# Performance work log

Measured on AMD Instinct MI355X. Metric: run time of the kernel, lower is better.

## Reference

```python
import jax, jax.numpy as jnp
import numpy as np
from jax import lax

DN = ('NCHW', 'OIHW', 'NCHW')
NUM_CODES = 8192


def _conv(x, w, b):
    # Conv2d(k=4, s=2, p=1)
    y = lax.conv_general_dilated(x, w, (2, 2), ((1, 1), (1, 1)), dimension_numbers=DN)
    return y + b[None, :, None, None]


def _convT(x, w, b):
    # ConvTranspose2d(k=4, s=2, p=1) as lhs-dilated conv; kernel already in equivalent OIHW layout
    y = lax.conv_general_dilated(x, w, (1, 1), ((2, 2), (2, 2)), lhs_dilation=(2, 2), dimension_numbers=DN)
    return y + b[None, :, None, None]


def _aff(x, s, b):
    # eval-mode BatchNorm folded to per-channel affine
    return x * s[None, :, None, None] + b[None, :, None, None]


def _forward(x, ew1, eb1, bn1s, bn1b, ew2, eb2, bn2s, bn2b, ew3, eb3, bn3s, bn3b, ew4, eb4, embed, cluster_size, dw1, db1, dbn1s, dbn1b, dw2, db2, dbn2s, dbn2b, dw3, db3, dbn3s, dbn3b, dw4, db4):
    sg = lax.stop_gradient
    embed = sg(embed)          # codebook is a torch buffer -> no grad
    cluster_size = sg(cluster_size)
    relu = jax.nn.relu
    # ---- Encoder: 4 stride-2 convs ----
    h = relu(_aff(_conv(x, ew1, eb1), bn1s, bn1b))
    h = relu(_aff(_conv(h, ew2, eb2), bn2s, bn2b))
    h = relu(_aff(_conv(h, ew3, eb3), bn3s, bn3b))
    z = _conv(h, ew4, eb4)                       # [B, D, G, G]
    zt = jnp.transpose(z, (0, 2, 3, 1))          # [B, G, G, D]
    D = zt.shape[-1]
    flat = zt.reshape(-1, D)                     # [N, D]
    N = flat.shape[0]
    # ---- VQ: pairwise squared distance + argmin codebook lookup ----
    dist = (flat * flat).sum(1, keepdims=True) - 2.0 * (flat @ embed.T) + (embed * embed).sum(1)[None, :]
    soft = jax.nn.softmax(-dist, axis=-1)        # temperature = 1.0
    codes = jnp.argmin(dist, axis=1)             # [N]
    zq = embed[codes]                            # [N, D]
    commitment_loss = jnp.mean((flat - sg(zq)) ** 2)
    codebook_loss = jnp.mean((zq - sg(flat)) ** 2)
    avg_soft = soft.mean(0)
    usage_entropy = -(avg_soft * jnp.log(avg_soft + 1e-10)).sum()
    diversity_loss = -usage_entropy / float(np.log(NUM_CODES))
    zq_st = flat + sg(zq - flat)                 # straight-through estimator
    zq_grid = jnp.transpose(zq_st.reshape(zt.shape), (0, 3, 1, 2))  # [B, D, G, G]
    # ---- Decoder: 4 stride-2 transposed convs ----
    h = relu(_aff(_convT(zq_grid, dw1, db1), dbn1s, dbn1b))
    h = relu(_aff(_convT(h, dw2, db2), dbn2s, dbn2b))
    h = relu(_aff(_convT(h, dw3, db3), dbn3s, dbn3b))
    recon = jax.nn.sigmoid(_convT(h, dw4, db4))
    recon_loss = jnp.mean((recon - x) ** 2)
    # ---- usage stats (no-grad in torch) ----
    hard_avg = jnp.zeros(NUM_CODES, flat.dtype).at[codes].add(1.0) / N
    perplexity = jnp.exp(-(hard_avg * jnp.log(hard_avg + 1e-10)).sum())
    active_codes = (cluster_size > 1).sum()
    codes_grid = codes.reshape(zt.shape[:-1])
    return (recon, recon_loss, codes_grid, zq_grid, commitment_loss, codebook_loss, diversity_loss, usage_entropy, perplexity, active_codes)


def setup_inputs() -> dict:
    keys = iter(jax.random.split(jax.random.key(0), 64))
    def randn(shape, s=1.0):
        return jax.random.normal(next(keys), shape, jnp.float32) * s
    def randu(shape):
        return jax.random.uniform(next(keys), shape, dtype=jnp.float32)
    B, H = 32, 256
    return {
        'x': randu((B, 1, H, H)),
        'ew1': randn((64, 1, 4, 4), 0.25), 'eb1': randn((64,), 0.1),
        'bn1s': randu((64,)), 'bn1b': randn((64,), 0.1),
        'ew2': randn((64, 64, 4, 4), 0.03), 'eb2': randn((64,), 0.1),
        'bn2s': randu((64,)), 'bn2b': randn((64,), 0.1),
        'ew3': randn((128, 64, 4, 4), 0.03), 'eb3': randn((128,), 0.1),
        'bn3s': randu((128,)), 'bn3b': randn((128,), 0.1),
        'ew4': randn((64, 128, 4, 4), 0.02), 'eb4': randn((64,), 0.1),
        'embed': randn((8192, 64), 0.5),
        'cluster_size': jnp.ones((8192,), jnp.float32),
        'dw1': randn((128, 64, 4, 4), 0.03), 'db1': randn((128,), 0.1),
        'dbn1s': randu((128,)), 'dbn1b': randn((128,), 0.1),
        'dw2': randn((64, 128, 4, 4), 0.02), 'db2': randn((64,), 0.1),
        'dbn2s': randu((64,)), 'dbn2b': randn((64,), 0.1),
        'dw3': randn((64, 64, 4, 4), 0.03), 'db3': randn((64,), 0.1),
        'dbn3s': randu((64,)), 'dbn3b': randn((64,), 0.1),
        'dw4': randn((1, 64, 4, 4), 0.03), 'db4': randn((1,), 0.1),
    }


def reference(x, ew1, eb1, bn1s, bn1b, ew2, eb2, bn2s, bn2b, ew3, eb3, bn3s, bn3b, ew4, eb4, embed, cluster_size, dw1, db1, dbn1s, dbn1b, dw2, db2, dbn2s, dbn2b, dw3, db3, dbn3s, dbn3b, dw4, db4):
    return _forward(x, ew1, eb1, bn1s, bn1b, ew2, eb2, bn2s, bn2b, ew3, eb3, bn3s, bn3b, ew4, eb4, embed, cluster_size, dw1, db1, dbn1s, dbn1b, dw2, db2, dbn2s, dbn2b, dw3, db3, dbn3s, dbn3b, dw4, db4)
```

## Files before the change

kernel.cpp:

```cpp
#include <hip/hip_runtime.h>
#include <cstdint>
#include <cstddef>


#define DEVI __device__ __forceinline__

typedef short  short8 __attribute__((ext_vector_type(8)));
typedef __bf16 bf16x8 __attribute__((ext_vector_type(8)));
typedef float  f32x16 __attribute__((ext_vector_type(16)));

DEVI f32x16 MFMA(bf16x8 a, bf16x8 b, f32x16 c){
  return __builtin_amdgcn_mfma_f32_32x32x16_bf16(a, b, c, 0, 0, 0);
}

DEVI ushort f2bf(float f){
  unsigned u = __float_as_uint(f);
  unsigned r = (u + 0x7FFFu + ((u >> 16) & 1u)) >> 16;
  return (ushort)r;
}
DEVI float bf2f(ushort h){ return __uint_as_float(((unsigned)h) << 16); }

union U8 { short8 s; bf16x8 b; };
DEVI bf16x8 ldg8u(const ushort* p){
  U8 u; u.s = *(const short8*)p; return u.b;
}

DEVI float wred64(float v){
  #pragma unroll
  for (int off=32; off>0; off>>=1) v += __shfl_down(v, off, 64);
  return v;
}

#define O_RECON     0
#define O_RLOSS     2097152
#define O_CODES     2097153
#define O_ZQ        2105345
#define O_COMMIT    2629633
#define O_CB        2629634
#define O_DIV       2629635
#define O_UE        2629636
#define O_PERP      2629637
#define O_ACT       2629638

#define WS_R1       0ull
#define A3H_OFF     0ull
#define A3M_OFF     8912896ull
#define A3L_OFF     17825792ull
#define PP_OFF      33554432ull
#define MT_OFF      37748736ull
#define PARTA_OFF   41943040ull
#define A2H_OFF     134217728ull
#define A2M_OFF     151519232ull
#define A2L_OFF     168820736ull
#define EH_OFF      134217728ull
#define EM_OFF      135266304ull
#define EL_OFF      136314880ull
#define FH_OFF      137363456ull
#define FM_OFF      138412032ull
#define FL_OFF      139460608ull
#define D2H_OFF     134217728ull
#define D2L_OFF     151519232ull
#define D1H_OFF     168820736ull
#define D1L_OFF     177733632ull
#define WS_FLAT     186646528ull
#define WS_ZQP      188743680ull
#define WS_WT       191102976ull
#define WT_E2       (WS_WT)
#define WT_E3       (WT_E2 + 393216ull)
#define WT_E4       (WT_E3 + 786432ull)
#define WT_D1       (WT_E4 + 786432ull)
#define WT_D2       (WT_D1 + 524288ull)
#define WT_D3       (WT_D2 + 524288ull)
#define WS_W4       (WT_D3 + 262144ull)
#define WS_STATS    (WS_W4 + 4096ull)
#define ST_RMP      (WS_STATS)
#define ST_CNT      (ST_RMP + 65536ull)
#define ST_AVGS     (ST_CNT + 32768ull)
#define ST_ROWZI    (ST_AVGS + 32768ull)
#define ST_CODESQ   (ST_ROWZI + 32768ull)
#define ST_LOSS     (ST_CODESQ + 32768ull)
#define ST_ROWM     (ST_LOSS + 32768ull)

DEVI void wsplit_body(int i, const float* src, ushort* dh, ushort* dm,
                      ushort* dl, int OC, int CIN, int isT, int three)
{
  if (i >= 16*OC*CIN) return;
  int cin = i % CIN; int t = i / CIN; int oc = t % OC; int tap = t / OC;
  int st;
  if (isT){
    int pq = tap>>2, ab = tap&3;
    int p = pq>>1, q = pq&1, a = ab>>1, b = ab&1;
    st = (p + 2*a)*4 + (q + 2*b);
  } else st = tap;
  float v = src[((size_t)oc*CIN + cin)*16 + st];
  ushort h = f2bf(v); float r = v - bf2f(h);
  if (three){
    ushort m = f2bf(r); float r2 = r - bf2f(m);
    dm[i] = m; dl[i] = f2bf(r2);
  } else {
    dl[i] = f2bf(r);
  }
  dh[i] = h;
}

DEVI void zpad_body(int i, unsigned* b0, unsigned* b1, unsigned* b2,
                    int rows, int Wp, int cwords)
{
  int total = rows*2*cwords;
  if (i >= total) return;
  int pos = i / cwords, cw = i % cwords;
  int row = pos >> 1, side = pos & 1;
  size_t w = ((size_t)row*Wp + (side ? (Wp-1) : 0))*cwords + cw;
  b0[w] = 0u;
  if (b1) b1[w] = 0u;
  if (b2) b2[w] = 0u;
}

__global__ __launch_bounds__(256) void k_prep(
    const float* __restrict__ ew2, const float* __restrict__ ew3,
    const float* __restrict__ ew4, const float* __restrict__ dw1,
    const float* __restrict__ dw2, const float* __restrict__ dw3,
    const float* __restrict__ dw4,
    ushort* wE2h, ushort* wE2m, ushort* wE2l,
    ushort* wE3h, ushort* wE3m, ushort* wE3l,
    ushort* wE4h, ushort* wE4m, ushort* wE4l,
    ushort* wD1h, ushort* wD1l, ushort* wD2h, ushort* wD2l,
    ushort* wD3h, ushort* wD3l, float* w4,
    unsigned* A2h, unsigned* A2m, unsigned* A2l,
    unsigned* zqPh, unsigned* zqPl,
    unsigned int* cnt, unsigned long long* rmp, float* loss)
{
  int b = blockIdx.x, tid = threadIdx.x;
  if (b < 32){
    int i = b*256 + tid;
    if (i < 8192){ cnt[i]=0u; rmp[i]=0xFFFFFFFFFFFFFFFFull; }
    if (i < 8) loss[i]=0.f;
  } else if (b < 288){
    wsplit_body((b-32)*256 + tid, ew2, wE2h, wE2m, wE2l, 64, 64, 0, 1);
  } else if (b < 800){
    wsplit_body((b-288)*256 + tid, ew3, wE3h, wE3m, wE3l, 128, 64, 0, 1);
  } else if (b < 1312){
    wsplit_body((b-800)*256 + tid, ew4, wE4h, wE4m, wE4l, 64, 128, 0, 1);
  } else if (b < 1824){
    wsplit_body((b-1312)*256 + tid, dw1, wD1h, nullptr, wD1l, 128, 64, 1, 0);
  } else if (b < 2336){
    wsplit_body((b-1824)*256 + tid, dw2, wD2h, nullptr, wD2l, 64, 128, 1, 0);
  } else if (b < 2592){
    wsplit_body((b-2336)*256 + tid, dw3, wD3h, nullptr, wD3l, 64, 64, 1, 0);
  } else if (b < 2596){
    int i = (b-2592)*256 + tid;
    if (i < 1024){
      int c = i & 63; int t16 = i >> 6;
      int pq = t16 >> 2, ab = t16 & 3;
      int p = pq>>1, q = pq&1, a = ab>>1, bb = ab&1;
      w4[i] = dw4[(size_t)c*16 + (p+2*a)*4 + (q+2*bb)];
    }
  } else if (b < 3108){
    zpad_body((b-2596)*256 + tid, A2h, A2m, A2l, 32*64, 66, 32);
  } else {
    zpad_body((b-3108)*256 + tid, zqPh, zqPl, nullptr, 32*16, 18, 32);
  }
}

__global__ __launch_bounds__(256) void k_zpadA3(unsigned* b0, unsigned* b1,
                                                unsigned* b2)
{
  zpad_body(blockIdx.x*256 + threadIdx.x, b0, b1, b2, 32*32, 34, 64);
}

__global__ __launch_bounds__(256) void k_eprep(
    const float* __restrict__ embed,
    ushort* __restrict__ dh, ushort* __restrict__ dm, ushort* __restrict__ dl,
    float* __restrict__ codesq)
{
  int b = blockIdx.x;
  if (b < 2048){
    int i = b*256 + threadIdx.x;
    float v = embed[i];
    ushort h = f2bf(v); float r1 = v - bf2f(h);
    ushort m = f2bf(r1); float r2 = r1 - bf2f(m);
    dh[i] = h; dm[i] = m; dl[i] = f2bf(r2);
  } else {
    int j = (b-2048)*4 + (threadIdx.x>>6);
    int c = threadIdx.x & 63;
    float e = embed[(size_t)j*64 + c];
    float s = wred64(e*e);
    if (c==0) codesq[j] = s;
  }
}

__global__ __launch_bounds__(256) void enc_conv1(
    const float* __restrict__ x, const float* __restrict__ w,
    const float* __restrict__ cb_, const float* __restrict__ bns,
    const float* __restrict__ bnb, float* __restrict__ out)
{
  __shared__ __align__(16) float sIn[34][36];
  __shared__ __align__(16) float sW[64][16];
  int b = blockIdx.x;
  int t = b & 63, n = b >> 6;
  int ty = t >> 3, tx = t & 7;
  int oy0 = ty*16, ox0 = tx*16;
  int iy0 = 2*oy0 - 1, ix0 = 2*ox0 - 1;
  int tid = threadIdx.x;
  int spg = tid & 31, og = tid >> 5;
  int sy = spg >> 1, x0 = (spg & 1)*8;

  if (tid < 64){
    const float* wp = w + tid*16;
    *(float4*)&sW[tid][0]  = *(const float4*)(wp);
    *(float4*)&sW[tid][4]  = *(const float4*)(wp+4);
    *(float4*)&sW[tid][8]  = *(const float4*)(wp+8);
    *(float4*)&sW[tid][12] = *(const float4*)(wp+12);
  }
  for (int e = tid; e < 34*34; e += 256){
    int rr = e/34, cc = e%34;
    int iy = iy0+rr, ix = ix0+cc;
    float v = 0.f;
    if ((unsigned)iy < 256u && (unsigned)ix < 256u)
      v = x[(size_t)n*65536 + iy*256 + ix];
    sIn[rr][cc] = v;
  }
  __syncthreads();

  float acc[8][8];
  #pragma unroll
  for (int j=0;j<8;j++)
    #pragma unroll
    for (int xi=0;xi<8;xi++) acc[j][xi]=0.f;

  #pragma unroll
  for (int ky=0; ky<4; ky++){
    int riy = 2*sy + ky;
    float seg[20];
    #pragma unroll
    for (int i=0;i<5;i++){
      float4 v = *(const float4*)&sIn[riy][2*x0 + 4*i];
      seg[4*i+0]=v.x; seg[4*i+1]=v.y; seg[4*i+2]=v.z; seg[4*i+3]=v.w;
    }
    #pragma unroll
    for (int j=0;j<8;j++){
      float4 w4v = *(const float4*)&sW[og*8+j][ky*4];
      #pragma unroll
      for (int xi=0; xi<8; xi++){
        acc[j][xi] = fmaf(seg[2*xi+0], w4v.x,
                     fmaf(seg[2*xi+1], w4v.y,
                     fmaf(seg[2*xi+2], w4v.z,
                     fmaf(seg[2*xi+3], w4v.w, acc[j][xi]))));
      }
    }
  }

  float sc[8], sh[8];
  #pragma unroll
  for (int j=0;j<8;j++){
    int oc = og*8+j;
    sc[j] = bns[oc];
    sh[j] = fmaf(cb_[oc], sc[j], bnb[oc]);
  }
  int oy = oy0 + sy;
  #pragma unroll
  for (int xi=0; xi<8; xi++){
    int oxg = ox0 + x0 + xi;
    float* op = out + (((size_t)n*128 + oy)*128 + oxg)*64 + og*8;
    float4 q0, q1;
    q0.x = fmaxf(fmaf(acc[0][xi], sc[0], sh[0]), 0.f);
    q0.y = fmaxf(fmaf(acc[1][xi], sc[1], sh[1]), 0.f);
    q0.z = fmaxf(fmaf(acc[2][xi], sc[2], sh[2]), 0.f);
    q0.w = fmaxf(fmaf(acc[3][xi], sc[3], sh[3]), 0.f);
    q1.x = fmaxf(fmaf(acc[4][xi], sc[4], sh[4]), 0.f);
    q1.y = fmaxf(fmaf(acc[5][xi], sc[5], sh[5]), 0.f);
    q1.z = fmaxf(fmaf(acc[6][xi], sc[6], sh[6]), 0.f);
    q1.w = fmaxf(fmaf(acc[7][xi], sc[7], sh[7]), 0.f);
    *(float4*)op     = q0;
    *(float4*)(op+4) = q1;
  }
}

template<int CIN, int OC, int OUTW, int OUTH, int INW, int INH, bool XPAD,
         int INMODE, int OUTMODE>
__global__ __launch_bounds__(256) void enc_conv(
    const float* __restrict__ in,
    const ushort* __restrict__ aH, const ushort* __restrict__ aM,
    const ushort* __restrict__ aL,
    const ushort* __restrict__ wtH, const ushort* __restrict__ wtM,
    const ushort* __restrict__ wtL,
    const float* __restrict__ cb_, const float* __restrict__ bns,
    const float* __restrict__ bnb,
    float* __restrict__ outF,
    ushort* __restrict__ oH, ushort* __restrict__ oM, ushort* __restrict__ oL,
    int nOcg)
{
  constexpr int INWP  = (INMODE==1) ? (INW+2) : (XPAD ? (INW+2) : INW);
  constexpr int WP    = INW + 2;
  constexpr int NROWS = 64 / OUTW;
  constexpr int AELEM = NROWS * WP * CIN;
  constexpr int BCIN  = (CIN > 64) ? 64 : CIN;
  constexpr int BELEM = 64 * BCIN;
  constexpr int NCH   = CIN / BCIN;
  constexpr int NSTG  = 16 * NCH;
  constexpr int PFI   = BELEM / 8 / 256;

  __shared__ __align__(16) ushort sAh[AELEM], sAm[AELEM], sAl[AELEM];
  __shared__ __align__(16) ushort sBh[BELEM], sBm[BELEM], sBl[BELEM];

  int b = blockIdx.x;
  int ocg = b % nOcg; b /= nOcg;
  int yb  = b % (OUTH/NROWS); b /= (OUTH/NROWS);
  int n = b;
  int oy0 = yb * NROWS, oc0 = ocg * 64;

  int tid = threadIdx.x;
  int l = tid & 63, wave = tid >> 6;
  int wm = wave >> 1, wn = wave & 1;
  int r = l & 31, kp = l >> 5;
  int idx = wm*32 + r;
  int oy_off = idx / OUTW, ox = idx % OUTW;

  int pfoc[PFI], pfc8[PFI];
  #pragma unroll
  for (int it=0; it<PFI; it++){
    int c = tid + it*256;
    pfoc[it] = c / (BCIN/8);
    pfc8[it] = (c % (BCIN/8)) * 8;
  }
  short8 pf0[PFI], pf1[PFI], pf2[PFI];
  {
    #pragma unroll
    for (int it=0; it<PFI; it++){
      size_t off = ((size_t)oc0 + pfoc[it])*CIN + pfc8[it];
      pf0[it] = *(const short8*)(wtH + off);
      pf1[it] = *(const short8*)(wtM + off);
      pf2[it] = *(const short8*)(wtL + off);
    }
  }

  f32x16 acc0, acc1, acc2, acc3;
  #pragma unroll
  for (int i=0;i<16;i++){ acc0[i]=0.f; acc1[i]=0.f; acc2[i]=0.f; acc3[i]=0.f; }

  const size_t nbase = (size_t)n * INH * INWP * CIN;
  int sidx = 0;

  for (int ky = 0; ky < 4; ky++){
    __syncthreads();
    for (int c = tid; c < AELEM/8; c += 256){
      int j  = c / (WP*CIN/8);
      int rm = c % (WP*CIN/8);
      int lx = rm / (CIN/8);
      int c8 = (rm % (CIN/8)) * 8;
      int iy = 2*(oy0 + j) - 1 + ky;
      bool ok = (unsigned)iy < (unsigned)INH;
      unsigned off = (unsigned)(((j*WP + lx)*CIN + c8)*2) ^ ((((unsigned)lx>>1)&15u)<<4);
      if constexpr (INMODE == 0){
        int gx = XPAD ? lx : (lx - 1);
        if (!XPAD) ok = ok && ((unsigned)gx < (unsigned)INW);
        float4 v0 = {0,0,0,0}, v1 = {0,0,0,0};
        if (ok){
          const float* s = in + nbase + ((size_t)iy*INWP + gx)*CIN + c8;
          v0 = *(const float4*)s; v1 = *(const float4*)(s+4);
        }
        float vv[8] = {v0.x,v0.y,v0.z,v0.w,v1.x,v1.y,v1.z,v1.w};
        short8 hh, mm, ll;
        #pragma unroll
        for (int e=0;e<8;e++){
          ushort h = f2bf(vv[e]); float r1 = vv[e] - bf2f(h);
          ushort m = f2bf(r1);    float r2 = r1 - bf2f(m);
          hh[e] = (short)h; mm[e] = (short)m; ll[e] = (short)f2bf(r2);
        }
        *(short8*)((char*)sAh + off) = hh;
        *(short8*)((char*)sAm + off) = mm;
        *(short8*)((char*)sAl + off) = ll;
      } else {
        short8 vh = {0,0,0,0,0,0,0,0}, vm = vh, vl = vh;
        if (ok){
          size_t s = nbase + ((size_t)iy*INWP + lx)*CIN + c8;
          vh = *(const short8*)(aH + s);
          vm = *(const short8*)(aM + s);
          vl = *(const short8*)(aL + s);
        }
        *(short8*)((char*)sAh + off) = vh;
        *(short8*)((char*)sAm + off) = vm;
        *(short8*)((char*)sAl + off) = vl;
      }
    }
    for (int kx = 0; kx < 4; kx++){
      for (int chi = 0; chi < NCH; chi++){
        int ch = chi * BCIN;
        __syncthreads();
        #pragma unroll
        for (int it=0; it<PFI; it++){
          unsigned off = (unsigned)((pfoc[it]*BCIN + pfc8[it])*2)
                         ^ (((unsigned)pfoc[it]&15u)<<4);
          *(short8*)((char*)sBh + off) = pf0[it];
          *(short8*)((char*)sBm + off) = pf1[it];
          *(short8*)((char*)sBl + off) = pf2[it];
        }
        __syncthreads();
        if (sidx + 1 < NSTG){
          int ns = sidx + 1;
          int ntap = ns / NCH, nchi = ns % NCH;
          #pragma unroll
          for (int it=0; it<PFI; it++){
            size_t off = ((size_t)ntap*OC + oc0 + pfoc[it])*CIN
                         + nchi*BCIN + pfc8[it];
            pf0[it] = *(const short8*)(wtH + off);
            pf1[it] = *(const short8*)(wtM + off);
            pf2[it] = *(const short8*)(wtL + off);
          }
        }
        sidx++;
        int lx = 2*ox + kx;
        unsigned asw  = ((((unsigned)lx>>1)&15u)<<4);
        unsigned alin = (unsigned)(((oy_off*WP + lx)*CIN)*2);
        int ocl = wn*32 + r;
        unsigned bsw  = (((unsigned)ocl&15u)<<4);
        unsigned blin = (unsigned)((ocl*BCIN)*2);
        #pragma unroll
        for (int ct = 0; ct < BCIN/16; ct++){
          unsigned kbA = (unsigned)((ch + ct*16 + kp*8)*2);
          unsigned kbB = (unsigned)((ct*16 + kp*8)*2);
          unsigned ao = (alin + kbA) ^ asw;
          unsigned bo = (blin + kbB) ^ bsw;
          bf16x8 ah = *(const bf16x8*)((char*)sAh + ao);
          bf16x8 am = *(const bf16x8*)((char*)sAm + ao);
          bf16x8 al = *(const bf16x8*)((char*)sAl + ao);
          bf16x8 bh = *(const bf16x8*)((char*)sBh + bo);
          bf16x8 bm = *(const bf16x8*)((char*)sBm + bo);
          bf16x8 bl = *(const bf16x8*)((char*)sBl + bo);
          acc0 = MFMA(ah, bh, acc0);
          acc1 = MFMA(ah, bm, acc1);
          acc2 = MFMA(am, bh, acc2);
          acc3 = MFMA(ah, bl, acc3);
          acc0 = MFMA(am, bm, acc0);
          acc1 = MFMA(al, bh, acc1);
        }
      }
    }
  }
  {
    int oce = oc0 + wn*32 + r;
    if constexpr (OUTMODE == 1){
      float cbv = cb_[oce];
      #pragma unroll
      for (int q = 0; q < 16; q++){
        int rowt = (q&3) + 8*(q>>2) + 4*kp;
        int m = wm*32 + rowt;
        int oyg = oy0 + m / OUTW;
        int oxg = m % OUTW;
        size_t row = (size_t)n*256 + oyg*16 + oxg;
        float v = (acc0[q] + acc1[q]) + (acc2[q] + acc3[q]) + cbv;
        outF[row*64 + oce] = v;
        ushort h = f2bf(v); float r1 = v - bf2f(h);
        ushort mm = f2bf(r1); float r2 = r1 - bf2f(mm);
        oH[row*64 + oce] = h;
        oM[row*64 + oce] = mm;
        oL[row*64 + oce] = f2bf(r2);
      }
    } else {
      float s1 = bns[oce];
      float s2 = fmaf(cb_[oce], s1, bnb[oce]);
      #pragma unroll
      for (int q = 0; q < 16; q++){
        int rowt = (q&3) + 8*(q>>2) + 4*kp;
        int m = wm*32 + rowt;
        int oyg = oy0 + m / OUTW;
        int oxg = m % OUTW;
        size_t pbase = (((size_t)n*OUTH + oyg)*(OUTW+2) + oxg + 1)*OC + oce;
        float v = fmaxf(fmaf((acc0[q] + acc1[q]) + (acc2[q] + acc3[q]), s1, s2), 0.f);
        ushort h = f2bf(v); float r1 = v - bf2f(h);
        ushort mm = f2bf(r1); float r2 = r1 - bf2f(mm);
        oH[pbase] = h;
        oM[pbase] = mm;
        oL[pbase] = f2bf(r2);
      }
    }
  }
}

DEVI float rmp_minval(unsigned long long v){
  unsigned skey = (unsigned)(v >> 32);
  unsigned u = (skey & 0x80000000u) ? (skey ^ 0x80000000u) : ~skey;
  return __uint_as_float(u);
}

__global__ __launch_bounds__(256) void vq_min(
    const ushort* __restrict__ fH, const ushort* __restrict__ fM,
    const ushort* __restrict__ fL,
    const ushort* __restrict__ eH, const ushort* __restrict__ eM,
    const ushort* __restrict__ eL,
    const float* __restrict__ codesq,
    unsigned long long* __restrict__ rmp,
    float* __restrict__ Pp, float* __restrict__ Mt)
{
  __shared__ __align__(16) ushort sAh[128*64], sAm[128*64], sAl[128*64];
  int cblk = blockIdx.x & 63, fblk = blockIdx.x >> 6;
  int code0 = cblk*128, f0 = fblk*128;
  int tid = threadIdx.x, l = tid&63, wave = tid>>6;
  int wm = wave>>1, wn = wave&1, r = l&31, kp = l>>5;

  for (int c = tid; c < 1024; c += 256){
    int rr = c >> 3, c8 = (c & 7)*8;
    size_t s = (size_t)(code0+rr)*64 + c8;
    unsigned off = (unsigned)((rr*64 + c8)*2) ^ (((unsigned)rr&15u)<<4);
    *(short8*)((char*)sAh + off) = *(const short8*)(eH + s);
    *(short8*)((char*)sAm + off) = *(const short8*)(eM + s);
    *(short8*)((char*)sAl + off) = *(const short8*)(eL + s);
  }
  __syncthreads();

  f32x16 acc[2][2];
  #pragma unroll
  for (int mt=0;mt<2;mt++)
    #pragma unroll
    for (int nt=0;nt<2;nt++)
      #pragma unroll
      for (int i=0;i<16;i++) acc[mt][nt][i]=0.f;

  #pragma unroll
  for (int ks=0; ks<4; ks++){
    unsigned kb = (unsigned)((ks*16 + kp*8)*2);
    int ko = ks*16 + kp*8;
    bf16x8 Ah[2],Am[2],Al[2],Bh[2],Bm[2],Bl[2];
    #pragma unroll
    for (int mt=0;mt<2;mt++){
      int rowi = wm*64 + mt*32 + r;
      unsigned o = ((unsigned)(rowi*128) + kb) ^ (((unsigned)rowi&15u)<<4);
      Ah[mt] = *(const bf16x8*)((char*)sAh + o);
      Am[mt] = *(const bf16x8*)((char*)sAm + o);
      Al[mt] = *(const bf16x8*)((char*)sAl + o);
    }
    #pragma unroll
    for (int nt=0;nt<2;nt++){
      int coli = f0 + wn*64 + nt*32 + r;
      size_t bo = (size_t)coli*64 + ko;
      Bh[nt] = ldg8u(fH + bo);
      Bm[nt] = ldg8u(fM + bo);
      Bl[nt] = ldg8u(fL + bo);
    }
    #pragma unroll
    for (int mt=0;mt<2;mt++)
      #pragma unroll
      for (int nt=0;nt<2;nt++){
        acc[mt][nt] = MFMA(Ah[mt], Bh[nt], acc[mt][nt]);
        acc[mt][nt] = MFMA(Ah[mt], Bm[nt], acc[mt][nt]);
        acc[mt][nt] = MFMA(Am[mt], Bh[nt], acc[mt][nt]);
        acc[mt][nt] = MFMA(Ah[mt], Bl[nt], acc[mt][nt]);
        acc[mt][nt] = MFMA(Am[mt], Bm[nt], acc[mt][nt]);
        acc[mt][nt] = MFMA(Al[mt], Bh[nt], acc[mt][nt]);
      }
  }

  float cqv[2][16];
  #pragma unroll
  for (int mt=0; mt<2; mt++)
    #pragma unroll
    for (int g=0; g<4; g++){
      float4 cv = *(const float4*)(codesq + code0 + wm*64 + mt*32 + 8*g + 4*kp);
      cqv[mt][4*g+0]=cv.x; cqv[mt][4*g+1]=cv.y;
      cqv[mt][4*g+2]=cv.z; cqv[mt][4*g+3]=cv.w;
    }

  #pragma unroll
  for (int nt=0; nt<2; nt++){
    int col = f0 + wn*64 + nt*32 + r;
    unsigned long long kmin = 0xFFFFFFFFFFFFFFFFull;
    #pragma unroll
    for (int mt=0; mt<2; mt++)
      #pragma unroll
      for (int q=0; q<16; q++){
        float d = cqv[mt][q] - 2.f*acc[mt][nt][q];
        int code = code0 + wm*64 + mt*32 + (q&3) + 8*(q>>2) + 4*kp;
        unsigned u = __float_as_uint(d);
        unsigned sgn = (unsigned)((int)u >> 31);
        unsigned skey = u ^ (sgn | 0x80000000u);
        unsigned long long key = (((unsigned long long)skey)<<32) | (unsigned)code;
        if (key < kmin) kmin = key;
      }
    unsigned long long o2 = __shfl_xor(kmin, 32, 64);
    if (o2 < kmin) kmin = o2;
    float mloc = rmp_minval(kmin);
    float p = 0.f;
    #pragma unroll
    for (int mt=0; mt<2; mt++)
      #pragma unroll
      for (int q=0; q<16; q++){
        float d = cqv[mt][q] - 2.f*acc[mt][nt][q];
        p += __expf(mloc - d);
      }
    p += __shfl_xor(p, 32, 64);
    if (kp == 0){
      atomicMin(&rmp[col], kmin);
      size_t pidx = (size_t)col*128 + (size_t)cblk*2 + wm;
      Pp[pidx] = p;
      Mt[pidx] = mloc;
    }
  }
}

__global__ __launch_bounds__(256) void k_rowz2(
    const unsigned long long* __restrict__ rmp,
    const float* __restrict__ Pp, const float* __restrict__ Mt,
    float* __restrict__ rowzi, float* __restrict__ rowm)
{
  int row = blockIdx.x*256 + threadIdx.x;
  float mg = rmp_minval(rmp[row]);
  const float* pp = Pp + (size_t)row*128;
  const float* mt = Mt + (size_t)row*128;
  float z = 0.f;
  for (int t = 0; t < 128; t++)
    z = fmaf(__expf(mg - mt[t]), pp[t], z);
  rowzi[row] = 1.f / z;
  rowm[row] = mg;
}

__global__ __launch_bounds__(256) void vq_avg(
    const ushort* __restrict__ fH, const ushort* __restrict__ fM,
    const ushort* __restrict__ fL,
    const ushort* __restrict__ eH, const ushort* __restrict__ eM,
    const ushort* __restrict__ eL,
    const float* __restrict__ codesq,
    const float* __restrict__ rowm,
    const float* __restrict__ rowzi,
    float* __restrict__ partA)
{
  __shared__ __align__(16) ushort sAh[128*64], sAm[128*64], sAl[128*64];
  __shared__ float colbuf[128];
  int cb = blockIdx.x & 63, rb = blockIdx.x >> 6;
  int row0 = rb*128, c0 = cb*128;
  int tid = threadIdx.x, l = tid&63, wave = tid>>6;
  int wm = wave>>1, wn = wave&1, r = l&31, kp = l>>5;

  if (tid < 128) colbuf[tid] = 0.f;

  for (int c = tid; c < 1024; c += 256){
    int rr = c >> 3, c8 = (c & 7)*8;
    size_t s = (size_t)(row0+rr)*64 + c8;
    unsigned off = (unsigned)((rr*64 + c8)*2) ^ (((unsigned)rr&15u)<<4);
    *(short8*)((char*)sAh + off) = *(const short8*)(fH + s);
    *(short8*)((char*)sAm + off) = *(const short8*)(fM + s);
    *(short8*)((char*)sAl + off) = *(const short8*)(fL + s);
  }
  __syncthreads();

  f32x16 acc[2][2];
  #pragma unroll
  for (int mt=0;mt<2;mt++)
    #pragma unroll
    for (int nt=0;nt<2;nt++)
      #pragma unroll
      for (int i=0;i<16;i++) acc[mt][nt][i]=0.f;

  #pragma unroll
  for (int ks=0; ks<4; ks++){
    unsigned kb = (unsigned)((ks*16 + kp*8)*2);
    int ko = ks*16 + kp*8;
    bf16x8 Ah[2],Am[2],Al[2],Bh[2],Bm[2],Bl[2];
    #pragma unroll
    for (int mt=0;mt<2;mt++){
      int rowi = wm*64 + mt*32 + r;
      unsigned o = ((unsigned)(rowi*128) + kb) ^ (((unsigned)rowi&15u)<<4);
      Ah[mt] = *(const bf16x8*)((char*)sAh + o);
      Am[mt] = *(const bf16x8*)((char*)sAm + o);
      Al[mt] = *(const bf16x8*)((char*)sAl + o);
    }
    #pragma unroll
    for (int nt=0;nt<2;nt++){
      int coli = c0 + wn*64 + nt*32 + r;
      size_t bo = (size_t)coli*64 + ko;
      Bh[nt] = ldg8u(eH + bo);
      Bm[nt] = ldg8u(eM + bo);
      Bl[nt] = ldg8u(eL + bo);
    }
    #pragma unroll
    for (int mt=0;mt<2;mt++)
      #pragma unroll
      for (int nt=0;nt<2;nt++){
        acc[mt][nt] = MFMA(Ah[mt], Bh[nt], acc[mt][nt]);
        acc[mt][nt] = MFMA(Ah[mt], Bm[nt], acc[mt][nt]);
        acc[mt][nt] = MFMA(Am[mt], Bh[nt], acc[mt][nt]);
        acc[mt][nt] = MFMA(Ah[mt], Bl[nt], acc[mt][nt]);
        acc[mt][nt] = MFMA(Am[mt], Bm[nt], acc[mt][nt]);
        acc[mt][nt] = MFMA(Al[mt], Bh[nt], acc[mt][nt]);
      }
  }

  float cq[2];
  cq[0] = codesq[c0 + wn*64 + r];
  cq[1] = codesq[c0 + wn*64 + 32 + r];
  float colacc[2] = {0.f, 0.f};
  #pragma unroll
  for (int mt=0; mt<2; mt++){
    #pragma unroll
    for (int q=0; q<16; q++){
      int rowt = (q&3) + 8*(q>>2) + 4*kp;
      int grow = row0 + wm*64 + mt*32 + rowt;
      float mi = rowm[grow];
      float zi = rowzi[grow];
      #pragma unroll
      for (int nt=0; nt<2; nt++){
        float d = cq[nt] - 2.f*acc[mt][nt][q];
        colacc[nt] = fmaf(__expf(mi - d), zi, colacc[nt]);
      }
    }
  }
  #pragma unroll
  for (int nt=0; nt<2; nt++){
    float o = __shfl_xor(colacc[nt], 32, 64);
    colacc[nt] += o;
    if (l < 32) atomicAdd(&colbuf[wn*64 + nt*32 + r], colacc[nt]);
  }
  __syncthreads();
  if (tid < 128)
    partA[(size_t)rb*8192 + c0 + tid] = colbuf[tid];
}

__global__ __launch_bounds__(256) void k_avgred(const float* __restrict__ partA,
                                                float* __restrict__ avgs)
{
  int j = blockIdx.x*256 + threadIdx.x;
  float s = 0.f;
  for (int rb = 0; rb < 64; rb++)
    s += partA[(size_t)rb*8192 + j];
  avgs[j] = s;
}

__global__ __launch_bounds__(256) void vq_post(
    const float* __restrict__ flat, const float* __restrict__ embed,
    const unsigned long long* __restrict__ rmp,
    float* __restrict__ out_codes, float* __restrict__ out_zq,
    ushort* __restrict__ zqPh, ushort* __restrict__ zqPl,
    float* __restrict__ loss, unsigned int* __restrict__ cnt,
    unsigned* __restrict__ d1h, unsigned* __restrict__ d1l,
    unsigned* __restrict__ d2h, unsigned* __restrict__ d2l)
{
  int blk = blockIdx.x;
  if (blk >= 2048){
    int zb = blk - 2048;
    if (zb < 512) zpad_body(zb*256 + threadIdx.x, d1h, d1l, nullptr, 32*32, 34, 64);
    else zpad_body((zb-512)*256 + threadIdx.x, d2h, d2l, nullptr, 32*64, 66, 32);
    return;
  }
  int r = blk*4 + (threadIdx.x>>6);
  int c = threadIdx.x & 63;
  unsigned j = (unsigned)(rmp[r] & 0xFFFFFFFFull);
  float e = embed[(size_t)j*64 + c];
  float f = flat[(size_t)r*64 + c];
  int n = r>>8, rem = r&255, gy = rem>>4, gx = rem&15;
  out_zq[(((size_t)n*64 + c)*16 + gy)*16 + gx] = e;
  ushort h = f2bf(e);
  size_t pz = (((size_t)n*16 + gy)*18 + gx + 1)*64 + c;
  zqPh[pz] = h; zqPl[pz] = f2bf(e - bf2f(h));
  float d = f - e;
  float s2 = wred64(d*d);
  if (c==0){
    out_codes[r] = (float)j;
    atomicAdd(cnt + j, 1u);
    atomicAdd(loss + 1, s2);
  }
}

template<int CIN, int OC, int SW, int SH, bool OUTPAD, int OMODE, int NPAR>
__global__ __launch_bounds__(256) void dec_convT_m(
    const ushort* __restrict__ inH, const ushort* __restrict__ inL,
    const ushort* __restrict__ wtH, const ushort* __restrict__ wtL,
    const float* __restrict__ db, const float* __restrict__ bns,
    const float* __restrict__ bnb,
    ushort* __restrict__ oH, ushort* __restrict__ oL, int nOcg)
{
  constexpr int TR    = 64 / SW;
  constexpr int NRA   = TR + ((NPAR==4) ? 2 : 1);
  constexpr int WPin  = SW + 2;
  constexpr int AELEM = NRA * WPin * CIN;
  constexpr int OUTH  = 2*SH;
  constexpr int OW    = OUTPAD ? (2*SW+2) : (2*SW);

  __shared__ __align__(16) ushort sAh[AELEM], sAl[AELEM];

  int b = blockIdx.x;
  int p_blk = 0;
  if (NPAR == 2){ p_blk = b & 1; b >>= 1; }
  int ocg = b % nOcg; b /= nOcg;
  int tb = b % (SH/TR); b /= (SH/TR);
  int n = b;
  int t0 = tb * TR, oc0 = ocg * 64;
  const int ROWBASE = (NPAR==4) ? -1 : (p_blk - 1);

  int tid = threadIdx.x, l = tid&63, wave = tid>>6;
  int wm = wave>>1, wn = wave&1;
  int r = l&31, kp = l>>5;
  int idx = wm*32 + r;
  int t_off = idx / SW, s = idx % SW;
  int ocl = oc0 + wn*32 + r;

  float bn_s1 = bns[ocl];
  float bn_s2 = fmaf(db[ocl], bn_s1, bnb[ocl]);

  for (int c = tid; c < AELEM/8; c += 256){
    int j  = c / (WPin*CIN/8);
    int rm = c % (WPin*CIN/8);
    int lx = rm / (CIN/8);
    int c8 = (rm % (CIN/8)) * 8;
    int giy = t0 + ROWBASE + j;
    bool ok = (unsigned)giy < (unsigned)SH;
    short8 vh = {0,0,0,0,0,0,0,0}, vl = {0,0,0,0,0,0,0,0};
    if (ok){
      size_t sidx = (((size_t)n*SH + giy)*WPin + lx)*CIN + c8;
      vh = *(const short8*)(inH + sidx);
      vl = *(const short8*)(inL + sidx);
    }
    unsigned off = (unsigned)(((j*WPin + lx)*CIN + c8)*2) ^ (((unsigned)lx&15u)<<4);
    *(short8*)((char*)sAh + off) = vh;
    *(short8*)((char*)sAl + off) = vl;
  }
  __syncthreads();

  for (int pr = 0; pr < NPAR; pr++){
    int p2 = (NPAR==4) ? (pr>>1) : p_blk;
    int q2 = (NPAR==4) ? (pr&1)  : pr;
    int par = p2*2 + q2;

    f32x16 acc0, acc1, acc2;
    #pragma unroll
    for (int i=0;i<16;i++){ acc0[i]=0.f; acc1[i]=0.f; acc2[i]=0.f; }

    for (int ab = 0; ab < 4; ab++){
      int a = ab>>1, bb = ab&1;
      int rs = t_off + ((NPAR==4) ? (p2 + a) : a);
      int lx = s + q2 + bb;
      unsigned asw  = (((unsigned)lx&15u)<<4);
      unsigned alin = (unsigned)(((rs*WPin + lx)*CIN)*2);
      size_t brow = ((size_t)(par*4 + ab)*OC + ocl)*CIN;
      #pragma unroll
      for (int ct = 0; ct < CIN/16; ct++){
        int ko = ct*16 + kp*8;
        unsigned ao = (alin + (unsigned)(ko*2)) ^ asw;
        bf16x8 ah = *(const bf16x8*)((char*)sAh + ao);
        bf16x8 al = *(const bf16x8*)((char*)sAl + ao);
        bf16x8 bh = ldg8u(wtH + brow + ko);
        bf16x8 bl = ldg8u(wtL + brow + ko);
        acc0 = MFMA(ah, bh, acc0);
        acc1 = MFMA(ah, bl, acc1);
        acc2 = MFMA(al, bh, acc2);
      }
    }

    #pragma unroll
    for (int q = 0; q < 16; q++){
      int rowt = (q&3) + 8*(q>>2) + 4*kp;
      int m = wm*32 + rowt;
      int y  = 2*(t0 + m/SW) + p2;
      int xs = m % SW;
      int xp = OUTPAD ? (2*xs + q2 + 1) : (2*xs + q2);
      size_t base = (((size_t)n*OUTH + y)*OW + xp)*OC + ocl;
      float v = fmaxf(fmaf(acc0[q] + acc1[q] + acc2[q], bn_s1, bn_s2), 0.f);
      ushort h = f2bf(v);
      oH[base] = h;
      if constexpr (OMODE == 0){
        oL[base] = f2bf(v - bf2f(h));
      }
    }
  }
}

__global__ __launch_bounds__(256) void dec_convT4(
    const ushort* __restrict__ d3, const float* __restrict__ w4,
    const float* __restrict__ db4, const float* __restrict__ xref,
    float* __restrict__ recon, float* __restrict__ loss)
{
  __shared__ __align__(16) float sT[10*10*68];
  __shared__ __align__(16) float sWt[16*64];
  __shared__ float red[4];
  int b = blockIdx.x;
  int t = b & 255, n = b >> 8;
  int ty = t >> 4, tx = t & 15;
  int y0 = ty*16, x0 = tx*16;
  int r0 = y0/2 - 1, c0 = x0/2 - 1;
  int tid = threadIdx.x;

  *(float4*)&sWt[tid*4] = *(const float4*)(w4 + tid*4);

  const ushort* base = d3 + (size_t)n*128*128*64;
  for (int e = tid; e < 800; e += 256){
    int rr = e/80; int rem = e%80; int cc = rem/8; int c8 = (rem%8)*8;
    int gr = r0+rr, gc = c0+cc;
    short8 v = {0,0,0,0,0,0,0,0};
    if ((unsigned)gr<128u && (unsigned)gc<128u)
      v = *(const short8*)(base + ((size_t)gr*128+gc)*64 + c8);
    float* dst = &sT[(rr*10+cc)*68 + c8];
    float4 f0, f1;
    f0.x = bf2f((ushort)v[0]); f0.y = bf2f((ushort)v[1]);
    f0.z = bf2f((ushort)v[2]); f0.w = bf2f((ushort)v[3]);
    f1.x = bf2f((ushort)v[4]); f1.y = bf2f((ushort)v[5]);
    f1.z = bf2f((ushort)v[6]); f1.w = bf2f((ushort)v[7]);
    *(float4*)dst     = f0;
    *(float4*)(dst+4) = f1;
  }
  __syncthreads();

  int sy = tid>>4, sx = tid&15;
  int p = sy&1, q = sx&1;
  int lr0 = (sy>>1)+p, lc0 = (sx>>1)+q;
  int par = p*2+q;
  float4 a4 = {0,0,0,0};
  #pragma unroll
  for (int a=0;a<2;a++){
    #pragma unroll
    for (int bb=0;bb<2;bb++){
      const float* ip = &sT[((lr0+a)*10 + lc0+bb)*68];
      const float* wp = &sWt[(par*4+a*2+bb)*64];
      #pragma unroll
      for (int c=0;c<64;c+=4){
        float4 v  = *(const float4*)(ip+c);
        float4 wv = *(const float4*)(wp+c);
        a4.x = fmaf(v.x, wv.x, a4.x);
        a4.y = fmaf(v.y, wv.y, a4.y);
        a4.z = fmaf(v.z, wv.z, a4.z);
        a4.w = fmaf(v.w, wv.w, a4.w);
      }
    }
  }
  float acc = (a4.x + a4.y) + (a4.z + a4.w);
  float v = acc + db4[0];
  float rcn = 1.f/(1.f + __expf(-v));
  int y = y0+sy, x = x0+sx;
  size_t oi = (size_t)n*65536 + (size_t)y*256 + x;
  recon[oi] = rcn;
  float d = rcn - xref[oi];
  float s2 = wred64(d*d);
  if ((tid & 63)==0) red[tid>>6] = s2;
  __syncthreads();
  if (tid==0) atomicAdd(loss + 0, red[0]+red[1]+red[2]+red[3]);
}

__global__ __launch_bounds__(256) void k_final(
    const float* __restrict__ avgs, const unsigned int* __restrict__ cnt,
    const float* __restrict__ cluster, const float* __restrict__ loss,
    float* __restrict__ dout)
{
  __shared__ float red[3][4];
  int tid = threadIdx.x;
  float e1=0.f, e2=0.f, ac=0.f;
  for (int j=tid; j<8192; j+=256){
    float a = avgs[j] * (1.f/8192.f);
    e1 += a * __logf(a + 1e-10f);
    float h = (float)cnt[j] * (1.f/8192.f);
    e2 += h * __logf(h + 1e-10f);
    ac += (cluster[j] > 1.f) ? 1.f : 0.f;
  }
  e1 = wred64(e1); e2 = wred64(e2); ac = wred64(ac);
  int wv = tid >> 6;
  if ((tid & 63)==0){ red[0][wv]=e1; red[1][wv]=e2; red[2][wv]=ac; }
  __syncthreads();
  if (tid==0){
    float s1 = red[0][0]+red[0][1]+red[0][2]+red[0][3];
    float s2 = red[1][0]+red[1][1]+red[1][2]+red[1][3];
    float s3 = red[2][0]+red[2][1]+red[2][2]+red[2][3];
    float ue = -s1;
    dout[O_RLOSS]  = loss[0] * (1.f/2097152.f);
    float cc = loss[1] * (1.f/524288.f);
    dout[O_COMMIT] = cc;
    dout[O_CB]     = cc;
    dout[O_DIV]    = -ue / 9.010913347279288f;
    dout[O_UE]     = ue;
    dout[O_PERP]   = __expf(-s2);
    dout[O_ACT]    = s3;
  }
}

extern "C" void kernel_launch(void* const* d_in, const int* in_sizes, int n_in,
                              void* d_out, int out_size, void* d_ws, size_t ws_size,
                              hipStream_t stream)
{
  (void)in_sizes; (void)n_in; (void)out_size; (void)ws_size;
  const float* x     = (const float*)d_in[0];
  const float* ew1   = (const float*)d_in[1];
  const float* eb1   = (const float*)d_in[2];
  const float* bn1s  = (const float*)d_in[3];
  const float* bn1b  = (const float*)d_in[4];
  const float* ew2   = (const float*)d_in[5];
  const float* eb2   = (const float*)d_in[6];
  const float* bn2s  = (const float*)d_in[7];
  const float* bn2b  = (const float*)d_in[8];
  const float* ew3   = (const float*)d_in[9];
  const float* eb3   = (const float*)d_in[10];
  const float* bn3s  = (const float*)d_in[11];
  const float* bn3b  = (const float*)d_in[12];
  const float* ew4   = (const float*)d_in[13];
  const float* eb4   = (const float*)d_in[14];
  const float* embed = (const float*)d_in[15];
  const float* clsz  = (const float*)d_in[16];
  const float* dw1   = (const float*)d_in[17];
  const float* db1   = (const float*)d_in[18];
  const float* dbn1s = (const float*)d_in[19];
  const float* dbn1b = (const float*)d_in[20];
  const float* dw2   = (const float*)d_in[21];
  const float* db2   = (const float*)d_in[22];
  const float* dbn2s = (const float*)d_in[23];
  const float* dbn2b = (const float*)d_in[24];
  const float* dw3   = (const float*)d_in[25];
  const float* db3   = (const float*)d_in[26];
  const float* dbn3s = (const float*)d_in[27];
  const float* dbn3b = (const float*)d_in[28];
  const float* dw4   = (const float*)d_in[29];
  const float* db4   = (const float*)d_in[30];

  float* out = (float*)d_out;
  uint8_t* wsb = (uint8_t*)d_ws;

  float*  A1   = (float*)(wsb + WS_R1);
  ushort* D3b  = (ushort*)(wsb + WS_R1);
  ushort* A3h  = (ushort*)(wsb + A3H_OFF);
  ushort* A3m  = (ushort*)(wsb + A3M_OFF);
  ushort* A3l  = (ushort*)(wsb + A3L_OFF);
  float*  Pp   = (float*)(wsb + PP_OFF);
  float*  Mt   = (float*)(wsb + MT_OFF);
  float*  partA= (float*)(wsb + PARTA_OFF);
  ushort* A2h  = (ushort*)(wsb + A2H_OFF);
  ushort* A2m  = (ushort*)(wsb + A2M_OFF);
  ushort* A2l  = (ushort*)(wsb + A2L_OFF);
  ushort* eH   = (ushort*)(wsb + EH_OFF);
  ushort* eM   = (ushort*)(wsb + EM_OFF);
  ushort* eL   = (ushort*)(wsb + EL_OFF);
  ushort* fH   = (ushort*)(wsb + FH_OFF);
  ushort* fM   = (ushort*)(wsb + FM_OFF);
  ushort* fL   = (ushort*)(wsb + FL_OFF);
  ushort* D1h  = (ushort*)(wsb + D1H_OFF);
  ushort* D1l  = (ushort*)(wsb + D1L_OFF);
  ushort* D2h  = (ushort*)(wsb + D2H_OFF);
  ushort* D2l  = (ushort*)(wsb + D2L_OFF);
  float*  flat = (float*)(wsb + WS_FLAT);
  ushort* zqPh = (ushort*)(wsb + WS_ZQP);
  ushort* zqPl = (ushort*)(wsb + WS_ZQP + 1179648ull);

  ushort* wE2h = (ushort*)(wsb + WT_E2);
  ushort* wE2m = wE2h + 65536;  ushort* wE2l = wE2m + 65536;
  ushort* wE3h = (ushort*)(wsb + WT_E3);
  ushort* wE3m = wE3h + 131072; ushort* wE3l = wE3m + 131072;
  ushort* wE4h = (ushort*)(wsb + WT_E4);
  ushort* wE4m = wE4h + 131072; ushort* wE4l = wE4m + 131072;
  ushort* wD1h = (ushort*)(wsb + WT_D1);
  ushort* wD1l = wD1h + 131072;
  ushort* wD2h = (ushort*)(wsb + WT_D2);
  ushort* wD2l = wD2h + 131072;
  ushort* wD3h = (ushort*)(wsb + WT_D3);
  ushort* wD3l = wD3h + 65536;
  float*  w4   = (float*)(wsb + WS_W4);

  unsigned long long* rmp = (unsigned long long*)(wsb + ST_RMP);
  unsigned int* cnt = (unsigned int*)(wsb + ST_CNT);
  float* avgs   = (float*)(wsb + ST_AVGS);
  float* rowzi  = (float*)(wsb + ST_ROWZI);
  float* codesq = (float*)(wsb + ST_CODESQ);
  float* loss   = (float*)(wsb + ST_LOSS);
  float* rowm   = (float*)(wsb + ST_ROWM);

  dim3 B(256);

  k_prep<<<3236, B, 0, stream>>>(
      ew2, ew3, ew4, dw1, dw2, dw3, dw4,
      wE2h, wE2m, wE2l, wE3h, wE3m, wE3l, wE4h, wE4m, wE4l,
      wD1h, wD1l, wD2h, wD2l, wD3h, wD3l, w4,
      (unsigned*)A2h, (unsigned*)A2m, (unsigned*)A2l,
      (unsigned*)zqPh, (unsigned*)zqPl,
      cnt, rmp, loss);

  enc_conv1<<<2048, B, 0, stream>>>(x, ew1, eb1, bn1s, bn1b, A1);
  enc_conv<64,64,64,64,128,128,false,0,0><<<2048, B, 0, stream>>>(
      A1, nullptr, nullptr, nullptr, wE2h, wE2m, wE2l, eb2, bn2s, bn2b,
      nullptr, A2h, A2m, A2l, 1);
  k_zpadA3<<<512, B, 0, stream>>>((unsigned*)A3h, (unsigned*)A3m, (unsigned*)A3l);
  enc_conv<64,128,32,32,64,64,true,1,0><<<1024, B, 0, stream>>>(
      nullptr, A2h, A2m, A2l, wE3h, wE3m, wE3l, eb3, bn3s, bn3b,
      nullptr, A3h, A3m, A3l, 2);
  k_eprep<<<4096, B, 0, stream>>>(embed, eH, eM, eL, codesq);
  enc_conv<128,64,16,16,32,32,true,1,1><<<128, B, 0, stream>>>(
      nullptr, A3h, A3m, A3l, wE4h, wE4m, wE4l, eb4, eb4, eb4,
      flat, fH, fM, fL, 1);

  vq_min<<<4096, B, 0, stream>>>(fH, fM, fL, eH, eM, eL, codesq, rmp, Pp, Mt);
  k_rowz2<<<32, B, 0, stream>>>(rmp, Pp, Mt, rowzi, rowm);
  vq_avg<<<4096, B, 0, stream>>>(fH, fM, fL, eH, eM, eL, codesq, rowm, rowzi, partA);
  k_avgred<<<32, B, 0, stream>>>(partA, avgs);

  vq_post<<<3072, B, 0, stream>>>(flat, embed, rmp, out + O_CODES, out + O_ZQ,
                                  zqPh, zqPl, loss, cnt,
                                  (unsigned*)D1h, (unsigned*)D1l,
                                  (unsigned*)D2h, (unsigned*)D2l);

  dec_convT_m<64,128,16,16,true,0,4><<<256, B, 0, stream>>>(
      zqPh, zqPl, wD1h, wD1l, db1, dbn1s, dbn1b, D1h, D1l, 2);
  dec_convT_m<128,64,32,32,true,0,2><<<1024, B, 0, stream>>>(
      D1h, D1l, wD2h, wD2l, db2, dbn2s, dbn2b, D2h, D2l, 1);
  dec_convT_m<64,64,64,64,false,2,4><<<2048, B, 0, stream>>>(
      D2h, D2l, wD3h, wD3l, db3, dbn3s, dbn3b, D3b, nullptr, 1);
  dec_convT4<<<8192, B, 0, stream>>>(D3b, w4, db4, x, out + O_RECON, loss);

  k_final<<<1, B, 0, stream>>>(avgs, cnt, clsz, loss, out);
}
```

Baseline: 906.4 us.

## Split encoder conv K-dimension across wave pairs with 512-thread blocks

The encoder conv kernel now launches 512 threads. Each pair of waves splits the 64-channel K chunk in half, and the two partial accumulators are reduced through shared memory that is aliased onto the weight staging buffer. Weight prefetch becomes one vector per thread, and A-tile loading is spread over twice as many threads. The intent is more waves in flight per block, so MFMA latency and load stalls are better hidden. The cost is an extra shared-memory reduction and sync, plus tighter register limits under launch_bounds(512).

```diff
diff --git a/kernel.cpp b/kernel.cpp
--- a/kernel.cpp
+++ b/kernel.cpp
@@ -278,7 +278,7 @@
 
 template<int CIN, int OC, int OUTW, int OUTH, int INW, int INH, bool XPAD,
          int INMODE, int OUTMODE>
-__global__ __launch_bounds__(256) void enc_conv(
+__global__ __launch_bounds__(512) void enc_conv(
     const float* __restrict__ in,
     const ushort* __restrict__ aH, const ushort* __restrict__ aM,
     const ushort* __restrict__ aL,
@@ -298,10 +298,15 @@
   constexpr int BELEM = 64 * BCIN;
   constexpr int NCH   = CIN / BCIN;
   constexpr int NSTG  = 16 * NCH;
-  constexpr int PFI   = BELEM / 8 / 256;
+  constexpr int NT    = 512;
+  constexpr int SCRSZ = (3*BELEM*2 > 4*64*16*4) ? 3*BELEM*2 : 4*64*16*4;
 
   __shared__ __align__(16) ushort sAh[AELEM], sAm[AELEM], sAl[AELEM];
-  __shared__ __align__(16) ushort sBh[BELEM], sBm[BELEM], sBl[BELEM];
+  __shared__ __align__(16) char sScr[SCRSZ];
+  ushort* sBh = (ushort*)sScr;
+  ushort* sBm = sBh + BELEM;
+  ushort* sBl = sBm + BELEM;
+  float*  sRed = (float*)sScr;
 
   int b = blockIdx.x;
   int ocg = b % nOcg; b /= nOcg;
@@ -311,27 +316,21 @@
 
   int tid = threadIdx.x;
   int l = tid & 63, wave = tid >> 6;
-  int wm = wave >> 1, wn = wave & 1;
+  int kh = wave & 1;
+  int wq = wave >> 1;
+  int wm = wq >> 1, wn = wq & 1;
   int r = l & 31, kp = l >> 5;
   int idx = wm*32 + r;
   int oy_off = idx / OUTW, ox = idx % OUTW;
 
-  int pfoc[PFI], pfc8[PFI];
-  #pragma unroll
-  for (int it=0; it<PFI; it++){
-    int c = tid + it*256;
-    pfoc[it] = c / (BCIN/8);
-    pfc8[it] = (c % (BCIN/8)) * 8;
-  }
-  short8 pf0[PFI], pf1[PFI], pf2[PFI];
+  int pfoc = tid / (BCIN/8);
+  int pfc8 = (tid % (BCIN/8)) * 8;
+  short8 pf0, pf1, pf2;
   {
-    #pragma unroll
-    for (int it=0; it<PFI; it++){
-      size_t off = ((size_t)oc0 + pfoc[it])*CIN + pfc8[it];
-      pf0[it] = *(const short8*)(wtH + off);
-      pf1[it] = *(const short8*)(wtM + off);
-      pf2[it] = *(const short8*)(wtL + off);
-    }
+    size_t off = ((size_t)oc0 + pfoc)*CIN + pfc8;
+    pf0 = *(const short8*)(wtH + off);
+    pf1 = *(const short8*)(wtM + off);
+    pf2 = *(const short8*)(wtL + off);
   }
 
   f32x16 acc0, acc1, acc2, acc3;
@@ -343,7 +342,7 @@
 
   for (int ky = 0; ky < 4; ky++){
     __syncthreads();
-    for (int c = tid; c < AELEM/8; c += 256){
+    for (int c = tid; c < AELEM/8; c += NT){
       int j  = c / (WP*CIN/8);
       int rm = c % (WP*CIN/8);
       int lx = rm / (CIN/8);
@@ -387,26 +386,21 @@
       for (int chi = 0; chi < NCH; chi++){
         int ch = chi * BCIN;
         __syncthreads();
-        #pragma unroll
-        for (int it=0; it<PFI; it++){
-          unsigned off = (unsigned)((pfoc[it]*BCIN + pfc8[it])*2)
-                         ^ (((unsigned)pfoc[it]&15u)<<4);
-          *(short8*)((char*)sBh + off) = pf0[it];
-          *(short8*)((char*)sBm + off) = pf1[it];
-          *(short8*)((char*)sBl + off) = pf2[it];
+        {
+          unsigned off = (unsigned)((pfoc*BCIN + pfc8)*2)
+                         ^ (((unsigned)pfoc&15u)<<4);
+          *(short8*)((char*)sBh + off) = pf0;
+          *(short8*)((char*)sBm + off) = pf1;
+          *(short8*)((char*)sBl + off) = pf2;
         }
         __syncthreads();
         if (sidx + 1 < NSTG){
           int ns = sidx + 1;
           int ntap = ns / NCH, nchi = ns % NCH;
-          #pragma unroll
-          for (int it=0; it<PFI; it++){
-            size_t off = ((size_t)ntap*OC + oc0 + pfoc[it])*CIN
-                         + nchi*BCIN + pfc8[it];
-            pf0[it] = *(const short8*)(wtH + off);
-            pf1[it] = *(const short8*)(wtM + off);
-            pf2[it] = *(const short8*)(wtL + off);
-          }
+          size_t off = ((size_t)ntap*OC + oc0 + pfoc)*CIN + nchi*BCIN + pfc8;
+          pf0 = *(const short8*)(wtH + off);
+          pf1 = *(const short8*)(wtM + off);
+          pf2 = *(const short8*)(wtL + off);
         }
         sidx++;
         int lx = 2*ox + kx;
@@ -416,7 +410,8 @@
         unsigned bsw  = (((unsigned)ocl&15u)<<4);
         unsigned blin = (unsigned)((ocl*BCIN)*2);
         #pragma unroll
-        for (int ct = 0; ct < BCIN/16; ct++){
+        for (int ct2 = 0; ct2 < 2; ct2++){
+          int ct = kh*2 + ct2;
           unsigned kbA = (unsigned)((ch + ct*16 + kp*8)*2);
           unsigned kbB = (unsigned)((ct*16 + kp*8)*2);
           unsigned ao = (alin + kbA) ^ asw;
@@ -437,7 +432,16 @@
       }
     }
   }
-  {
+  __syncthreads();
+  if (kh == 1){
+    float* dst = sRed + ((size_t)(wq*64 + l)*16);
+    #pragma unroll
+    for (int q = 0; q < 16; q++)
+      dst[q] = (acc0[q] + acc1[q]) + (acc2[q] + acc3[q]);
+  }
+  __syncthreads();
+  if (kh == 0){
+    const float* srcp = sRed + ((size_t)(wq*64 + l)*16);
     int oce = oc0 + wn*32 + r;
     if constexpr (OUTMODE == 1){
       float cbv = cb_[oce];
@@ -448,7 +452,7 @@
         int oyg = oy0 + m / OUTW;
         int oxg = m % OUTW;
         size_t row = (size_t)n*256 + oyg*16 + oxg;
-        float v = (acc0[q] + acc1[q]) + (acc2[q] + acc3[q]) + cbv;
+        float v = ((acc0[q] + acc1[q]) + (acc2[q] + acc3[q])) + srcp[q] + cbv;
         outF[row*64 + oce] = v;
         ushort h = f2bf(v); float r1 = v - bf2f(h);
         ushort mm = f2bf(r1); float r2 = r1 - bf2f(mm);
@@ -466,7 +470,8 @@
         int oyg = oy0 + m / OUTW;
         int oxg = m % OUTW;
         size_t pbase = (((size_t)n*OUTH + oyg)*(OUTW+2) + oxg + 1)*OC + oce;
-        float v = fmaxf(fmaf((acc0[q] + acc1[q]) + (acc2[q] + acc3[q]), s1, s2), 0.f);
+        float acc = ((acc0[q] + acc1[q]) + (acc2[q] + acc3[q])) + srcp[q];
+        float v = fmaxf(fmaf(acc, s1, s2), 0.f);
         ushort h = f2bf(v); float r1 = v - bf2f(h);
         ushort mm = f2bf(r1); float r2 = r1 - bf2f(mm);
         oH[pbase] = h;
@@ -1055,6 +1060,7 @@
   float* rowm   = (float*)(wsb + ST_ROWM);
 
   dim3 B(256);
+  dim3 B5(512);
 
   k_prep<<<3236, B, 0, stream>>>(
       ew2, ew3, ew4, dw1, dw2, dw3, dw4,
@@ -1065,15 +1071,15 @@
       cnt, rmp, loss);
 
   enc_conv1<<<2048, B, 0, stream>>>(x, ew1, eb1, bn1s, bn1b, A1);
-  enc_conv<64,64,64,64,128,128,false,0,0><<<2048, B, 0, stream>>>(
+  enc_conv<64,64,64,64,128,128,false,0,0><<<2048, B5, 0, stream>>>(
       A1, nullptr, nullptr, nullptr, wE2h, wE2m, wE2l, eb2, bn2s, bn2b,
       nullptr, A2h, A2m, A2l, 1);
   k_zpadA3<<<512, B, 0, stream>>>((unsigned*)A3h, (unsigned*)A3m, (unsigned*)A3l);
-  enc_conv<64,128,32,32,64,64,true,1,0><<<1024, B, 0, stream>>>(
+  enc_conv<64,128,32,32,64,64,true,1,0><<<1024, B5, 0, stream>>>(
       nullptr, A2h, A2m, A2l, wE3h, wE3m, wE3l, eb3, bn3s, bn3b,
       nullptr, A3h, A3m, A3l, 2);
   k_eprep<<<4096, B, 0, stream>>>(embed, eH, eM, eL, codesq);
-  enc_conv<128,64,16,16,32,32,true,1,1><<<128, B, 0, stream>>>(
+  enc_conv<128,64,16,16,32,32,true,1,1><<<128, B5, 0, stream>>>(
       nullptr, A3h, A3m, A3l, wE4h, wE4m, wE4l, eb4, eb4, eb4,
       flat, fH, fM, fL, 1);
 
```

Measured after the change: 935.7 us. 3.2% more time.
